# Kernel tuning notes

Hardware: AMD Instinct MI355X
Metric: run time of the kernel (lower is better)

The kernel has to match this reference:

```python
import jax, jax.numpy as jnp
import numpy as np

EMBED = 1024
HEADS = 16
HEAD_DIM = EMBED // HEADS


def setup_inputs() -> dict:
    key = jax.random.key(0)
    ks = jax.random.split(key, 11)
    B, S = 2, 2048
    scale = 1.0 / np.sqrt(EMBED)
    inp = {
        'Q': jax.random.normal(ks[0], (B, S, EMBED), jnp.float32),
        'K': jax.random.normal(ks[1], (B, S, EMBED), jnp.float32),
        'V': jax.random.normal(ks[2], (B, S, EMBED), jnp.float32),
        'Wq': jax.random.normal(ks[3], (EMBED, EMBED), jnp.float32) * scale,
        'bq': jnp.zeros((EMBED,), jnp.float32),
        'Wk': jax.random.normal(ks[4], (EMBED, EMBED), jnp.float32) * scale,
        'bk': jnp.zeros((EMBED,), jnp.float32),
        'Wv': jax.random.normal(ks[5], (EMBED, EMBED), jnp.float32) * scale,
        'bv': jnp.zeros((EMBED,), jnp.float32),
        'Wo': jax.random.normal(ks[6], (EMBED, EMBED), jnp.float32) * scale,
        'bo': jnp.zeros((EMBED,), jnp.float32),
    }
    return inp


def reference(Q, K, V, Wq, bq, Wk, bk, Wv, bv, Wo, bo):
    B, Sq, _ = Q.shape
    Sk = K.shape[1]
    # linear projections (torch nn.Linear: x @ W.T + b; here W stored as [in,out])
    q = Q @ Wq + bq
    k = K @ Wk + bk
    v = V @ Wv + bv
    # [B, H, S, D]
    q = q.reshape(B, Sq, HEADS, HEAD_DIM).transpose(0, 2, 1, 3)
    k = k.reshape(B, Sk, HEADS, HEAD_DIM).transpose(0, 2, 1, 3)
    v = v.reshape(B, Sk, HEADS, HEAD_DIM).transpose(0, 2, 1, 3)
    scores = jnp.einsum('bhqd,bhkd->bhqk', q, k) / jnp.sqrt(jnp.float32(HEAD_DIM))
    attn = jax.nn.softmax(scores, axis=-1)
    out = jnp.einsum('bhqk,bhkd->bhqd', attn, v)
    out = out.transpose(0, 2, 1, 3).reshape(B, Sq, EMBED)
    return out @ Wo + bo
```

## Files before the change

### kernel.cpp

```cpp
#include <hip/hip_runtime.h>

#define EMBED 1024
#define HEADS 16
#define HDIM  64
#define BATCH 2
#define SEQ   2048
#define MTOK  (BATCH*SEQ)

typedef _Float16 half_t;
typedef __attribute__((ext_vector_type(4))) float    f32x4;
typedef __attribute__((ext_vector_type(8))) _Float16 f16x8;
typedef __attribute__((ext_vector_type(4))) _Float16 f16x4;

#define MFMA16(a,b,c) __builtin_amdgcn_mfma_f32_16x16x32_f16(a,b,c,0,0,0)

#define GLOAD_LDS16(gp, lp)                                                     \
    __builtin_amdgcn_global_load_lds(                                           \
        (const __attribute__((address_space(1))) void*)(gp),                    \
        (__attribute__((address_space(3))) void*)(lp), 16, 0, 0)

#define QSCALE 0.18033688f

__global__ __launch_bounds__(256) void wt_kernel(const float* __restrict__ W0,
                                                 const float* __restrict__ W1,
                                                 const float* __restrict__ W2,
                                                 const float* __restrict__ W3,
                                                 half_t* __restrict__ T0,
                                                 half_t* __restrict__ T1,
                                                 half_t* __restrict__ T2,
                                                 half_t* __restrict__ T3)
{
    const int z = blockIdx.z;
    const float* W = (z == 0) ? W0 : (z == 1) ? W1 : (z == 2) ? W2 : W3;
    half_t* WT     = (z == 0) ? T0 : (z == 1) ? T1 : (z == 2) ? T2 : T3;

    __shared__ float tile[64][68];
    const int t  = threadIdx.x;
    const int n0 = blockIdx.x * 64;
    const int k0 = blockIdx.y * 64;
#pragma unroll
    for (int i = 0; i < 4; ++i) {
        int f = t + 256 * i;
        int r = f >> 4, c4 = (f & 15) << 2;
        float4 v = *(const float4*)(W + (size_t)(k0 + r) * EMBED + n0 + c4);
        tile[r][c4 + 0] = v.x; tile[r][c4 + 1] = v.y;
        tile[r][c4 + 2] = v.z; tile[r][c4 + 3] = v.w;
    }
    __syncthreads();
#pragma unroll
    for (int i = 0; i < 4; ++i) {
        int f = t + 256 * i;
        int nr = f >> 4, kc = (f & 15) << 2;
        f16x4 o;
        o[0] = (half_t)tile[kc + 0][nr];
        o[1] = (half_t)tile[kc + 1][nr];
        o[2] = (half_t)tile[kc + 2][nr];
        o[3] = (half_t)tile[kc + 3][nr];
        *(f16x4*)(WT + (size_t)(n0 + nr) * EMBED + k0 + kc) = o;
    }
}

__global__ __launch_bounds__(256) void conv_kernel(const float* __restrict__ S0,
                                                   const float* __restrict__ S1,
                                                   const float* __restrict__ S2,
                                                   half_t* __restrict__ D0,
                                                   half_t* __restrict__ D1,
                                                   half_t* __restrict__ D2)
{
    const int z = blockIdx.z;
    const float* S = (z == 0) ? S0 : (z == 1) ? S1 : S2;
    half_t* D      = (z == 0) ? D0 : (z == 1) ? D1 : D2;
    size_t idx = ((size_t)blockIdx.x * 256 + threadIdx.x) * 8;
    float4 v0 = *(const float4*)(S + idx);
    float4 v1 = *(const float4*)(S + idx + 4);
    f16x8 hv;
    hv[0] = (half_t)v0.x; hv[1] = (half_t)v0.y;
    hv[2] = (half_t)v0.z; hv[3] = (half_t)v0.w;
    hv[4] = (half_t)v1.x; hv[5] = (half_t)v1.y;
    hv[6] = (half_t)v1.z; hv[7] = (half_t)v1.w;
    *(f16x8*)(D + idx) = hv;
}

__global__ __launch_bounds__(256, 3) void proj3_kernel(const half_t* __restrict__ Aq,
                                                       const half_t* __restrict__ Ak,
                                                       const half_t* __restrict__ Av,
                                                       const half_t* __restrict__ Btq,
                                                       const half_t* __restrict__ Btk,
                                                       const half_t* __restrict__ Btv,
                                                       const float*  __restrict__ bq,
                                                       const float*  __restrict__ bk,
                                                       const float*  __restrict__ bv,
                                                       half_t* __restrict__ oq,
                                                       half_t* __restrict__ ok,
                                                       half_t* __restrict__ ov)
{
    const int z = blockIdx.z;
    const half_t* A    = (z == 0) ? Aq  : (z == 1) ? Ak  : Av;
    const half_t* Bt   = (z == 0) ? Btq : (z == 1) ? Btk : Btv;
    const float*  bias = (z == 0) ? bq  : (z == 1) ? bk  : bv;
    half_t*       out  = (z == 0) ? oq  : (z == 1) ? ok  : ov;

    __shared__ half_t As[128 * 64];
    __shared__ half_t Bs[128 * 64];
    const int tid = threadIdx.x, lane = tid & 63, g = lane >> 4, ln = lane & 15;
    const int w = tid >> 6, wm = w >> 1, wn = w & 1;
    const int n0 = blockIdx.x * 128, m0 = blockIdx.y * 128;
    const int srow8 = lane >> 3, schunk = lane & 7;

    f32x4 acc[4][4];
#pragma unroll
    for (int i = 0; i < 4; ++i)
#pragma unroll
        for (int j = 0; j < 4; ++j) acc[i][j] = (f32x4){0.f, 0.f, 0.f, 0.f};

    for (int kt = 0; kt < EMBED; kt += 64) {
#pragma unroll
        for (int i = 0; i < 4; ++i) {
            int row = (i * 4 + w) * 8 + srow8;
            GLOAD_LDS16(A  + (size_t)(m0 + row) * EMBED + kt + schunk * 8,
                        (char*)As + (i * 4 + w) * 1024);
            GLOAD_LDS16(Bt + (size_t)(n0 + row) * EMBED + kt + schunk * 8,
                        (char*)Bs + (i * 4 + w) * 1024);
        }
        __syncthreads();
#pragma unroll
        for (int k2 = 0; k2 < 2; ++k2) {
            f16x8 af[4], bf[4];
#pragma unroll
            for (int mi = 0; mi < 4; ++mi)
                af[mi] = *(const f16x8*)(As + (wm * 64 + mi * 16 + ln) * 64 + k2 * 32 + g * 8);
#pragma unroll
            for (int ni = 0; ni < 4; ++ni)
                bf[ni] = *(const f16x8*)(Bs + (wn * 64 + ni * 16 + ln) * 64 + k2 * 32 + g * 8);
#pragma unroll
            for (int mi = 0; mi < 4; ++mi)
#pragma unroll
                for (int ni = 0; ni < 4; ++ni)
                    acc[mi][ni] = MFMA16(af[mi], bf[ni], acc[mi][ni]);
        }
        __syncthreads();
    }

#pragma unroll
    for (int mi = 0; mi < 4; ++mi) {
#pragma unroll
        for (int ni = 0; ni < 4; ++ni) {
            int col = n0 + wn * 64 + ni * 16 + ln;
            float bb = bias[col];
            int h = col >> 6, d = col & 63;
            if (z == 2) {
                int row0 = m0 + wm * 64 + mi * 16 + g * 4;
                int b = row0 >> 11, s = row0 & 2047;
                f16x4 o4;
#pragma unroll
                for (int r = 0; r < 4; ++r)
                    o4[r] = (half_t)(acc[mi][ni][r] + bb);
                *(f16x4*)(out + ((size_t)(b * HEADS + h) * HDIM + d) * SEQ + s) = o4;
            } else {
#pragma unroll
                for (int r = 0; r < 4; ++r) {
                    int row = m0 + wm * 64 + mi * 16 + g * 4 + r;
                    int b = row >> 11, s = row & 2047;
                    float val = acc[mi][ni][r] + bb;
                    if (z == 0) val *= QSCALE;
                    out[((size_t)(b * HEADS + h) * SEQ + s) * HDIM + d] = (half_t)val;
                }
            }
        }
    }
}

__global__ __launch_bounds__(256, 4) void final_kernel(const half_t* __restrict__ A,
                                                       const half_t* __restrict__ Bt,
                                                       const float*  __restrict__ bias,
                                                       float* __restrict__ out)
{
    __shared__ half_t As[64 * 64];
    __shared__ half_t Bs[128 * 64];
    const int tid = threadIdx.x, lane = tid & 63, g = lane >> 4, ln = lane & 15;
    const int w = tid >> 6, wm = w >> 1, wn = w & 1;
    const int n0 = blockIdx.x * 128, m0 = blockIdx.y * 64;
    const int srow8 = lane >> 3, schunk = lane & 7;

    f32x4 acc[2][4];
#pragma unroll
    for (int i = 0; i < 2; ++i)
#pragma unroll
        for (int j = 0; j < 4; ++j) acc[i][j] = (f32x4){0.f, 0.f, 0.f, 0.f};

    for (int kt = 0; kt < EMBED; kt += 64) {
#pragma unroll
        for (int i = 0; i < 2; ++i) {
            int rg = i * 4 + w;
            GLOAD_LDS16(A + (size_t)(m0 + rg * 8 + srow8) * EMBED + kt + schunk * 8,
                        (char*)As + rg * 1024);
        }
#pragma unroll
        for (int i = 0; i < 4; ++i) {
            int rg = i * 4 + w;
            GLOAD_LDS16(Bt + (size_t)(n0 + rg * 8 + srow8) * EMBED + kt + schunk * 8,
                        (char*)Bs + rg * 1024);
        }
        __syncthreads();
#pragma unroll
        for (int k2 = 0; k2 < 2; ++k2) {
            f16x8 af[2], bf[4];
#pragma unroll
            for (int mi = 0; mi < 2; ++mi)
                af[mi] = *(const f16x8*)(As + (wm * 32 + mi * 16 + ln) * 64 + k2 * 32 + g * 8);
#pragma unroll
            for (int ni = 0; ni < 4; ++ni)
                bf[ni] = *(const f16x8*)(Bs + (wn * 64 + ni * 16 + ln) * 64 + k2 * 32 + g * 8);
#pragma unroll
            for (int mi = 0; mi < 2; ++mi)
#pragma unroll
                for (int ni = 0; ni < 4; ++ni)
                    acc[mi][ni] = MFMA16(af[mi], bf[ni], acc[mi][ni]);
        }
        __syncthreads();
    }
#pragma unroll
    for (int mi = 0; mi < 2; ++mi) {
#pragma unroll
        for (int ni = 0; ni < 4; ++ni) {
            int col = n0 + wn * 64 + ni * 16 + ln;
            float bb = bias[col];
#pragma unroll
            for (int r = 0; r < 4; ++r) {
                int row = m0 + wm * 32 + mi * 16 + g * 4 + r;
                out[(size_t)row * EMBED + col] = acc[mi][ni][r] + bb;
            }
        }
    }
}

__global__ __launch_bounds__(256, 2) void attn_kernel(const half_t* __restrict__ q,
                                                      const half_t* __restrict__ k,
                                                      const half_t* __restrict__ vt,
                                                      half_t* __restrict__ ao)
{
    __shared__ half_t Ks[64 * 64];
    __shared__ half_t Vs[64 * 64];
    __shared__ half_t Ps[4][32 * 72];
    const int tid = threadIdx.x, lane = tid & 63, g = lane >> 4, ln = lane & 15;
    const int w = tid >> 6;

    const int fid = blockIdx.x;
    const int j = fid & 7, t = fid >> 3;
    const int yhi = t >> 4, x = t & 15;
    const int bh = yhi * 8 + j;
    const int bb = bh >> 4, h = bh & 15;

    const half_t* qh = q  + (size_t)bh * SEQ * HDIM;
    const half_t* kh = k  + (size_t)bh * SEQ * HDIM;
    const half_t* vh = vt + (size_t)bh * HDIM * SEQ;
    const int qrow0 = x * 128 + w * 32;

    f16x8 qfrag[2][2];
#pragma unroll
    for (int mt = 0; mt < 2; ++mt)
#pragma unroll
        for (int kt = 0; kt < 2; ++kt)
            qfrag[mt][kt] = *(const f16x8*)(qh + (size_t)(qrow0 + mt * 16 + ln) * HDIM + kt * 32 + g * 8);

    f32x4 accO[2][4];
#pragma unroll
    for (int mt = 0; mt < 2; ++mt)
#pragma unroll
        for (int nt = 0; nt < 4; ++nt) accO[mt][nt] = (f32x4){0.f, 0.f, 0.f, 0.f};
    float lsum[2] = {0.f, 0.f};

    const int srow0 = tid >> 3;
    const int scol16 = tid & 7;

    {
        f16x8 rK[2], rV[2];
#pragma unroll
        for (int c = 0; c < 2; ++c) {
            int row = c * 32 + srow0;
            rK[c] = *(const f16x8*)(kh + (size_t)row * HDIM + scol16 * 8);
            rV[c] = *(const f16x8*)(vh + (size_t)row * SEQ + scol16 * 8);
        }
#pragma unroll
        for (int c = 0; c < 2; ++c) {
            int row = c * 32 + srow0;
            int off = row * 128 + ((scol16 * 16) ^ ((row & 7) << 4));
            *(f16x8*)((char*)Ks + off) = rK[c];
            *(f16x8*)((char*)Vs + off) = rV[c];
        }
    }
    __syncthreads();

    for (int kv = 0; kv < SEQ; kv += 64) {
        f32x4 accT[2][4];
#pragma unroll
        for (int mt = 0; mt < 2; ++mt)
#pragma unroll
            for (int kb = 0; kb < 4; ++kb) accT[mt][kb] = (f32x4){0.f, 0.f, 0.f, 0.f};
#pragma unroll
        for (int kt = 0; kt < 2; ++kt) {
            f16x8 kf[4];
#pragma unroll
            for (int kb = 0; kb < 4; ++kb) {
                int row = kb * 16 + ln;
                kf[kb] = *(const f16x8*)((char*)Ks + row * 128 + ((kt * 64 + g * 16) ^ ((row & 7) << 4)));
            }
            __builtin_amdgcn_s_setprio(1);
#pragma unroll
            for (int mt = 0; mt < 2; ++mt)
#pragma unroll
                for (int kb = 0; kb < 4; ++kb)
                    accT[mt][kb] = MFMA16(kf[kb], qfrag[mt][kt], accT[mt][kb]);
            __builtin_amdgcn_s_setprio(0);
        }

        const bool has_next = (kv + 64) < SEQ;
        f16x8 rK[2], rV[2];
        if (has_next) {
#pragma unroll
            for (int c = 0; c < 2; ++c) {
                int row = c * 32 + srow0;
                rK[c] = *(const f16x8*)(kh + (size_t)(kv + 64 + row) * HDIM + scol16 * 8);
                rV[c] = *(const f16x8*)(vh + (size_t)row * SEQ + kv + 64 + scol16 * 8);
            }
        }

#pragma unroll
        for (int mt = 0; mt < 2; ++mt) {
#pragma unroll
            for (int kb = 0; kb < 4; ++kb) {
                float p0 = __builtin_amdgcn_exp2f(accT[mt][kb][0]);
                float p1 = __builtin_amdgcn_exp2f(accT[mt][kb][1]);
                float p2 = __builtin_amdgcn_exp2f(accT[mt][kb][2]);
                float p3 = __builtin_amdgcn_exp2f(accT[mt][kb][3]);
                lsum[mt] += (p0 + p1) + (p2 + p3);
                f16x4 pv;
                pv[0] = (half_t)p0; pv[1] = (half_t)p1;
                pv[2] = (half_t)p2; pv[3] = (half_t)p3;
                *(f16x4*)(&Ps[w][(mt * 16 + ln) * 72 + kb * 16 + g * 4]) = pv;
            }
        }

#pragma unroll
        for (int kt = 0; kt < 2; ++kt) {
            f16x8 bf[4], ap[2];
#pragma unroll
            for (int nt = 0; nt < 4; ++nt) {
                int row = nt * 16 + ln;
                bf[nt] = *(const f16x8*)((char*)Vs + row * 128 + ((kt * 64 + g * 16) ^ ((row & 7) << 4)));
            }
#pragma unroll
            for (int mt = 0; mt < 2; ++mt)
                ap[mt] = *(const f16x8*)(&Ps[w][(mt * 16 + ln) * 72 + kt * 32 + g * 8]);
            __builtin_amdgcn_s_setprio(1);
#pragma unroll
            for (int mt = 0; mt < 2; ++mt)
#pragma unroll
                for (int nt = 0; nt < 4; ++nt)
                    accO[mt][nt] = MFMA16(ap[mt], bf[nt], accO[mt][nt]);
            __builtin_amdgcn_s_setprio(0);
        }

        if (has_next) {
            __syncthreads();
#pragma unroll
            for (int c = 0; c < 2; ++c) {
                int row = c * 32 + srow0;
                int off = row * 128 + ((scol16 * 16) ^ ((row & 7) << 4));
                *(f16x8*)((char*)Ks + off) = rK[c];
                *(f16x8*)((char*)Vs + off) = rV[c];
            }
            __syncthreads();
        }
    }

#pragma unroll
    for (int mt = 0; mt < 2; ++mt) {
        lsum[mt] += __shfl_xor(lsum[mt], 16);
        lsum[mt] += __shfl_xor(lsum[mt], 32);
    }

#pragma unroll
    for (int mt = 0; mt < 2; ++mt) {
#pragma unroll
        for (int r = 0; r < 4; ++r) {
            float linv = 1.0f / __shfl(lsum[mt], g * 4 + r);
            int srow_o = qrow0 + mt * 16 + g * 4 + r;
#pragma unroll
            for (int nt = 0; nt < 4; ++nt) {
                int d = nt * 16 + ln;
                ao[((size_t)(bb * SEQ + srow_o)) * EMBED + h * HDIM + d] =
                    (half_t)(accO[mt][nt][r] * linv);
            }
        }
    }
}

extern "C" void kernel_launch(void* const* d_in, const int* in_sizes, int n_in,
                              void* d_out, int out_size, void* d_ws, size_t ws_size,
                              hipStream_t stream)
{
    const float* Q  = (const float*)d_in[0];
    const float* K  = (const float*)d_in[1];
    const float* V  = (const float*)d_in[2];
    const float* Wq = (const float*)d_in[3];
    const float* bq = (const float*)d_in[4];
    const float* Wk = (const float*)d_in[5];
    const float* bk = (const float*)d_in[6];
    const float* Wv = (const float*)d_in[7];
    const float* bv = (const float*)d_in[8];
    const float* Wo = (const float*)d_in[9];
    const float* bo = (const float*)d_in[10];
    float* out = (float*)d_out;

    half_t* ws = (half_t*)d_ws;
    const size_t WSZ = (size_t)EMBED * EMBED;
    const size_t TSZ = (size_t)MTOK * EMBED;
    half_t* WqT = ws;
    half_t* WkT = WqT + WSZ;
    half_t* WvT = WkT + WSZ;
    half_t* WoT = WvT + WSZ;
    half_t* Qc  = WoT + WSZ;
    half_t* Kc  = Qc + TSZ;
    half_t* Vc  = Kc + TSZ;
    half_t* qf  = Vc + TSZ;
    half_t* kf  = qf + TSZ;
    half_t* vT  = kf + TSZ;
    half_t* ao  = vT + TSZ;

    dim3 blk(256);
    wt_kernel<<<dim3(16, 16, 4), blk, 0, stream>>>(Wq, Wk, Wv, Wo, WqT, WkT, WvT, WoT);
    conv_kernel<<<dim3(2048, 1, 3), blk, 0, stream>>>(Q, K, V, Qc, Kc, Vc);

    proj3_kernel<<<dim3(EMBED / 128, MTOK / 128, 3), blk, 0, stream>>>(
        Qc, Kc, Vc, WqT, WkT, WvT, bq, bk, bv, qf, kf, vT);

    attn_kernel<<<dim3(512), blk, 0, stream>>>(qf, kf, vT, ao);

    final_kernel<<<dim3(EMBED / 128, MTOK / 64), blk, 0, stream>>>(ao, WoT, bo, out);
}
```

Measured before the change: 125.4 us.

## Double-buffer K/V tiles in LDS with direct global-to-LDS loads

```diff
diff --git a/kernel.cpp b/kernel.cpp
--- a/kernel.cpp
+++ b/kernel.cpp
@@ -239,8 +239,8 @@
                                                       const half_t* __restrict__ vt,
                                                       half_t* __restrict__ ao)
 {
-    __shared__ half_t Ks[64 * 64];
-    __shared__ half_t Vs[64 * 64];
+    __shared__ half_t Ks[2][64 * 64];
+    __shared__ half_t Vs[2][64 * 64];
     __shared__ half_t Ps[4][32 * 72];
     const int tid = threadIdx.x, lane = tid & 63, g = lane >> 4, ln = lane & 15;
     const int w = tid >> 6;
@@ -270,28 +270,34 @@
         for (int nt = 0; nt < 4; ++nt) accO[mt][nt] = (f32x4){0.f, 0.f, 0.f, 0.f};
     float lsum[2] = {0.f, 0.f};
 
-    const int srow0 = tid >> 3;
-    const int scol16 = tid & 7;
-
-    {
-        f16x8 rK[2], rV[2];
-#pragma unroll
-        for (int c = 0; c < 2; ++c) {
-            int row = c * 32 + srow0;
-            rK[c] = *(const f16x8*)(kh + (size_t)row * HDIM + scol16 * 8);
-            rV[c] = *(const f16x8*)(vh + (size_t)row * SEQ + scol16 * 8);
-        }
-#pragma unroll
-        for (int c = 0; c < 2; ++c) {
-            int row = c * 32 + srow0;
-            int off = row * 128 + ((scol16 * 16) ^ ((row & 7) << 4));
-            *(f16x8*)((char*)Ks + off) = rK[c];
-            *(f16x8*)((char*)Vs + off) = rV[c];
-        }
+    const int e0 = w * 2;
+    const int lrow   = lane >> 3;
+    const int lchunk = (lane & 7) ^ lrow;
+
+#pragma unroll
+    for (int c = 0; c < 2; ++c) {
+        int e = e0 + c;
+        GLOAD_LDS16(kh + (size_t)(e * 8 + lrow) * HDIM + lchunk * 8,
+                    (char*)Ks[0] + e * 1024);
+        GLOAD_LDS16(vh + (size_t)(e * 8 + lrow) * SEQ + lchunk * 8,
+                    (char*)Vs[0] + e * 1024);
     }
     __syncthreads();
 
-    for (int kv = 0; kv < SEQ; kv += 64) {
+    for (int it = 0; it < SEQ / 64; ++it) {
+        const int cur = it & 1;
+        if (it + 1 < SEQ / 64) {
+            const int kvn = (it + 1) * 64;
+#pragma unroll
+            for (int c = 0; c < 2; ++c) {
+                int e = e0 + c;
+                GLOAD_LDS16(kh + (size_t)(kvn + e * 8 + lrow) * HDIM + lchunk * 8,
+                            (char*)Ks[cur ^ 1] + e * 1024);
+                GLOAD_LDS16(vh + (size_t)(e * 8 + lrow) * SEQ + kvn + lchunk * 8,
+                            (char*)Vs[cur ^ 1] + e * 1024);
+            }
+        }
+
         f32x4 accT[2][4];
 #pragma unroll
         for (int mt = 0; mt < 2; ++mt)
@@ -303,7 +309,7 @@
 #pragma unroll
             for (int kb = 0; kb < 4; ++kb) {
                 int row = kb * 16 + ln;
-                kf[kb] = *(const f16x8*)((char*)Ks + row * 128 + ((kt * 64 + g * 16) ^ ((row & 7) << 4)));
+                kf[kb] = *(const f16x8*)((char*)Ks[cur] + row * 128 + ((kt * 64 + g * 16) ^ ((row & 7) << 4)));
             }
             __builtin_amdgcn_s_setprio(1);
 #pragma unroll
@@ -312,17 +318,6 @@
                 for (int kb = 0; kb < 4; ++kb)
                     accT[mt][kb] = MFMA16(kf[kb], qfrag[mt][kt], accT[mt][kb]);
             __builtin_amdgcn_s_setprio(0);
-        }
-
-        const bool has_next = (kv + 64) < SEQ;
-        f16x8 rK[2], rV[2];
-        if (has_next) {
-#pragma unroll
-            for (int c = 0; c < 2; ++c) {
-                int row = c * 32 + srow0;
-                rK[c] = *(const f16x8*)(kh + (size_t)(kv + 64 + row) * HDIM + scol16 * 8);
-                rV[c] = *(const f16x8*)(vh + (size_t)row * SEQ + kv + 64 + scol16 * 8);
-            }
         }
 
 #pragma unroll
@@ -347,7 +342,7 @@
 #pragma unroll
             for (int nt = 0; nt < 4; ++nt) {
                 int row = nt * 16 + ln;
-                bf[nt] = *(const f16x8*)((char*)Vs + row * 128 + ((kt * 64 + g * 16) ^ ((row & 7) << 4)));
+                bf[nt] = *(const f16x8*)((char*)Vs[cur] + row * 128 + ((kt * 64 + g * 16) ^ ((row & 7) << 4)));
             }
 #pragma unroll
             for (int mt = 0; mt < 2; ++mt)
@@ -361,17 +356,7 @@
             __builtin_amdgcn_s_setprio(0);
         }
 
-        if (has_next) {
-            __syncthreads();
-#pragma unroll
-            for (int c = 0; c < 2; ++c) {
-                int row = c * 32 + srow0;
-                int off = row * 128 + ((scol16 * 16) ^ ((row & 7) << 4));
-                *(f16x8*)((char*)Ks + off) = rK[c];
-                *(f16x8*)((char*)Vs + off) = rV[c];
-            }
-            __syncthreads();
-        }
+        __syncthreads();
     }
 
 #pragma unroll
```

New measurement: 127.7 us. About the same (+1.8%).
